# Optimization experiments

Measured on AMD Instinct MI355X. Metric: run time of the kernel, lower is better.

Reference implementation:

```python
import jax, jax.numpy as jnp
import numpy as np

N, E, D_EMB, D_OUT, K = 4096, 131072, 128, 64, 3


def setup_inputs() -> dict:
    key = jax.random.key(0)
    k1, k2, k3, k4 = jax.random.split(key, 4)
    node_features = jax.random.normal(k1, (N, D_EMB), dtype=jnp.float32)
    edge_index = jax.random.randint(k2, (2, E), 0, N, dtype=jnp.int32)
    edge_weights = jax.random.uniform(k3, (E,), dtype=jnp.float32)
    # xavier_uniform-like init for Emb (shape [embdsize, nin])
    limit = float(np.sqrt(6.0 / (D_EMB + D_OUT)))
    Emb = jax.random.uniform(k4, (D_EMB, D_OUT), dtype=jnp.float32, minval=-limit, maxval=limit)
    return {"node_features": node_features, "Emb": Emb,
            "edge_index": edge_index, "edge_weights": edge_weights}


def reference(node_features, Emb, edge_index, edge_weights):
    # embedding: [N, embdsize] @ [embdsize, nin] -> [N, nin]
    x = node_features @ Emb
    n = x.shape[0]
    A = jnp.zeros((n, n), dtype=x.dtype).at[edge_index[0], edge_index[1]].set(edge_weights)
    # matrix_power(A, K) @ x  ==  K repeated A @ x (associativity), avoids forming A^K
    for _ in range(K):
        x = A @ x
    return x
```

## Files before the change

### kernel.cpp

```cpp
#include <hip/hip_runtime.h>
#include <stdint.h>


#define N_NODES 4096
#define D_EMB   128
#define D_OUT   64

#define CAP       128
#define CAP_SHIFT 7

__global__ void embed_kernel(const float* __restrict__ nf,
                             const float* __restrict__ emb,
                             float* __restrict__ x,
                             int* __restrict__ cnt) {
    int tid = blockIdx.x * blockDim.x + threadIdx.x;
    if (tid < N_NODES) cnt[tid] = 0;

    __shared__ float srow[4][D_EMB];
    int wave = threadIdx.x >> 6;
    int lane = threadIdx.x & 63;
    int row  = blockIdx.x * 4 + wave;
    srow[wave][lane]      = nf[row * D_EMB + lane];
    srow[wave][lane + 64] = nf[row * D_EMB + lane + 64];
    __syncthreads();
    float acc = 0.0f;
#pragma unroll 8
    for (int k = 0; k < D_EMB; ++k)
        acc = fmaf(srow[wave][k], emb[k * D_OUT + lane], acc);
    x[row * D_OUT + lane] = acc;
}

__global__ void scatter_kernel(const int* __restrict__ ei,
                               const float* __restrict__ ew, int E,
                               int* __restrict__ cnt,
                               int2* __restrict__ slots,
                               int* __restrict__ eids) {
    int e = blockIdx.x * blockDim.x + threadIdx.x;
    if (e >= E) return;
    int src = ei[e];
    int dst = ei[E + e];
    int idx = atomicAdd(&cnt[src], 1);
    if (idx < CAP) {
        int2 s;
        s.x = dst;
        s.y = __float_as_int(ew[e]);
        int p = (src << CAP_SHIFT) + idx;
        slots[p] = s;
        eids[p]  = e;
    }
}

__global__ void dedup_spmm_kernel(const int* __restrict__ cnt,
                                  int2* __restrict__ slots,
                                  const int* __restrict__ eids,
                                  const float* __restrict__ x,
                                  float* __restrict__ y) {
    __shared__ int   sdst[4][CAP];
    __shared__ int   seid[4][CAP];
    __shared__ float sw[4][CAP];

    int wave = threadIdx.x >> 6;
    int lane = threadIdx.x & 63;
    int row  = blockIdx.x * 4 + wave;
    int c = cnt[row];
    if (c > CAP) c = CAP;
    int2* s = slots + ((long)row << CAP_SHIFT);
    const int* se = eids + ((long)row << CAP_SHIFT);

#pragma unroll
    for (int half = 0; half < 2; ++half) {
        int i = lane + half * 64;
        if (i < c) {
            int2 si = s[i];
            sdst[wave][i] = si.x;
            sw[wave][i]   = __int_as_float(si.y);
            seid[wave][i] = se[i];
        }
    }
    __syncthreads();

#pragma unroll
    for (int half = 0; half < 2; ++half) {
        int i = lane + half * 64;
        if (i < c) {
            int d = sdst[wave][i], id = seid[wave][i];
            bool loser = false;
            for (int j = 0; j < c; ++j)
                loser |= (sdst[wave][j] == d) & (seid[wave][j] > id);
            if (loser) {
                sw[wave][i] = 0.0f;
                s[i].y = 0;
            }
        }
    }
    __syncthreads();

    float acc = 0.0f;
    int i = 0;
    for (; i + 4 <= c; i += 4) {
        float v0 = x[sdst[wave][i]     * D_OUT + lane];
        float v1 = x[sdst[wave][i + 1] * D_OUT + lane];
        float v2 = x[sdst[wave][i + 2] * D_OUT + lane];
        float v3 = x[sdst[wave][i + 3] * D_OUT + lane];
        acc = fmaf(sw[wave][i],     v0, acc);
        acc = fmaf(sw[wave][i + 1], v1, acc);
        acc = fmaf(sw[wave][i + 2], v2, acc);
        acc = fmaf(sw[wave][i + 3], v3, acc);
    }
    for (; i < c; ++i)
        acc = fmaf(sw[wave][i], x[sdst[wave][i] * D_OUT + lane], acc);
    y[row * D_OUT + lane] = acc;
}

__global__ void spmm_kernel(const int* __restrict__ cnt,
                            const int2* __restrict__ slots,
                            const float* __restrict__ x,
                            float* __restrict__ y) {
    int wave = threadIdx.x >> 6;
    int lane = threadIdx.x & 63;
    int row  = blockIdx.x * 4 + wave;
    int c = cnt[row];
    if (c > CAP) c = CAP;
    const int2* s = slots + ((long)row << CAP_SHIFT);
    float acc = 0.0f;
    int i = 0;
    for (; i + 4 <= c; i += 4) {
        int2 s0 = s[i], s1 = s[i + 1], s2 = s[i + 2], s3 = s[i + 3];
        float v0 = x[s0.x * D_OUT + lane];
        float v1 = x[s1.x * D_OUT + lane];
        float v2 = x[s2.x * D_OUT + lane];
        float v3 = x[s3.x * D_OUT + lane];
        acc = fmaf(__int_as_float(s0.y), v0, acc);
        acc = fmaf(__int_as_float(s1.y), v1, acc);
        acc = fmaf(__int_as_float(s2.y), v2, acc);
        acc = fmaf(__int_as_float(s3.y), v3, acc);
    }
    for (; i < c; ++i) {
        int2 si = s[i];
        acc = fmaf(__int_as_float(si.y), x[si.x * D_OUT + lane], acc);
    }
    y[row * D_OUT + lane] = acc;
}

extern "C" void kernel_launch(void* const* d_in, const int* in_sizes, int n_in,
                              void* d_out, int out_size, void* d_ws, size_t ws_size,
                              hipStream_t stream) {
    const float* nf  = (const float*)d_in[0];
    const float* emb = (const float*)d_in[1];
    const int*   ei  = (const int*)d_in[2];
    const float* ew  = (const float*)d_in[3];
    float* out = (float*)d_out;

    const int E = in_sizes[3];

    char* ws = (char*)d_ws;
    size_t o = 0;
    auto take = [&](size_t bytes) -> void* {
        void* p = ws + o;
        o += (bytes + 255) & ~(size_t)255;
        return p;
    };
    int*  cnt   = (int*)take((size_t)N_NODES * 4);
    int2* slots = (int2*)take((size_t)N_NODES * CAP * 8);
    int*  eids  = (int*)take((size_t)N_NODES * CAP * 4);
    float* x0   = (float*)take((size_t)N_NODES * D_OUT * 4);
    float* x1   = (float*)take((size_t)N_NODES * D_OUT * 4);

    const int TB = 256;
    const int EB = (E + TB - 1) / TB;
    const int NB = N_NODES / 4;

    embed_kernel<<<NB, TB, 0, stream>>>(nf, emb, x0, cnt);
    scatter_kernel<<<EB, TB, 0, stream>>>(ei, ew, E, cnt, slots, eids);
    dedup_spmm_kernel<<<NB, TB, 0, stream>>>(cnt, slots, eids, x0, x1);
    spmm_kernel<<<NB, TB, 0, stream>>>(cnt, slots, x1, x0);
    spmm_kernel<<<NB, TB, 0, stream>>>(cnt, slots, x0, out);
}
```

Before: 48.54 us.

## Fuse embed and scatter kernels, pack slots as int4, stage edges in LDS

Merges the embedding GEMM and the edge scatter into one launch by splitting block ranges, and moves the counter zeroing to a memset. Edge id is packed with dst and weight into a single int4 slot, so the separate eid array goes away. Both SpMM kernels now stage slot data into shared memory and unroll the gather by 8 for more memory-level parallelism. The trade-off is that slot storage doubles from 8 to 16 bytes per entry, which adds scatter write traffic, and the memset adds a launch.

```diff
diff --git a/kernel.cpp b/kernel.cpp
--- a/kernel.cpp
+++ b/kernel.cpp
@@ -9,50 +9,46 @@
 #define CAP       128
 #define CAP_SHIFT 7
 
-__global__ void embed_kernel(const float* __restrict__ nf,
-                             const float* __restrict__ emb,
-                             float* __restrict__ x,
-                             int* __restrict__ cnt) {
-    int tid = blockIdx.x * blockDim.x + threadIdx.x;
-    if (tid < N_NODES) cnt[tid] = 0;
-
-    __shared__ float srow[4][D_EMB];
-    int wave = threadIdx.x >> 6;
-    int lane = threadIdx.x & 63;
-    int row  = blockIdx.x * 4 + wave;
-    srow[wave][lane]      = nf[row * D_EMB + lane];
-    srow[wave][lane + 64] = nf[row * D_EMB + lane + 64];
-    __syncthreads();
-    float acc = 0.0f;
+__global__ void embed_scatter_kernel(const float* __restrict__ nf,
+                                     const float* __restrict__ emb,
+                                     float* __restrict__ x,
+                                     const int* __restrict__ ei,
+                                     const float* __restrict__ ew, int E,
+                                     int* __restrict__ cnt,
+                                     int4* __restrict__ slots) {
+    if (blockIdx.x < 1024) {
+        __shared__ float srow[4][D_EMB];
+        int wave = threadIdx.x >> 6;
+        int lane = threadIdx.x & 63;
+        int row  = blockIdx.x * 4 + wave;
+        float2 a = ((const float2*)(nf + (size_t)row * D_EMB))[lane];
+        srow[wave][2 * lane]     = a.x;
+        srow[wave][2 * lane + 1] = a.y;
+        __syncthreads();
+        float acc = 0.0f;
 #pragma unroll 8
-    for (int k = 0; k < D_EMB; ++k)
-        acc = fmaf(srow[wave][k], emb[k * D_OUT + lane], acc);
-    x[row * D_OUT + lane] = acc;
-}
-
-__global__ void scatter_kernel(const int* __restrict__ ei,
-                               const float* __restrict__ ew, int E,
-                               int* __restrict__ cnt,
-                               int2* __restrict__ slots,
-                               int* __restrict__ eids) {
-    int e = blockIdx.x * blockDim.x + threadIdx.x;
-    if (e >= E) return;
-    int src = ei[e];
-    int dst = ei[E + e];
-    int idx = atomicAdd(&cnt[src], 1);
-    if (idx < CAP) {
-        int2 s;
-        s.x = dst;
-        s.y = __float_as_int(ew[e]);
-        int p = (src << CAP_SHIFT) + idx;
-        slots[p] = s;
-        eids[p]  = e;
+        for (int k = 0; k < D_EMB; ++k)
+            acc = fmaf(srow[wave][k], emb[k * D_OUT + lane], acc);
+        x[row * D_OUT + lane] = acc;
+    } else {
+        int e = (blockIdx.x - 1024) * blockDim.x + threadIdx.x;
+        if (e >= E) return;
+        int src = ei[e];
+        int dst = ei[E + e];
+        int idx = atomicAdd(&cnt[src], 1);
+        if (idx < CAP) {
+            int4 s;
+            s.x = dst;
+            s.y = __float_as_int(ew[e]);
+            s.z = e;
+            s.w = 0;
+            slots[(src << CAP_SHIFT) + idx] = s;
+        }
     }
 }
 
 __global__ void dedup_spmm_kernel(const int* __restrict__ cnt,
-                                  int2* __restrict__ slots,
-                                  const int* __restrict__ eids,
+                                  int4* __restrict__ slots,
                                   const float* __restrict__ x,
                                   float* __restrict__ y) {
     __shared__ int   sdst[4][CAP];
@@ -64,17 +60,16 @@
     int row  = blockIdx.x * 4 + wave;
     int c = cnt[row];
     if (c > CAP) c = CAP;
-    int2* s = slots + ((long)row << CAP_SHIFT);
-    const int* se = eids + ((long)row << CAP_SHIFT);
+    int4* s = slots + ((long)row << CAP_SHIFT);
 
 #pragma unroll
     for (int half = 0; half < 2; ++half) {
         int i = lane + half * 64;
         if (i < c) {
-            int2 si = s[i];
+            int4 si = s[i];
             sdst[wave][i] = si.x;
             sw[wave][i]   = __int_as_float(si.y);
-            seid[wave][i] = se[i];
+            seid[wave][i] = si.z;
         }
     }
     __syncthreads();
@@ -89,7 +84,7 @@
                 loser |= (sdst[wave][j] == d) & (seid[wave][j] > id);
             if (loser) {
                 sw[wave][i] = 0.0f;
-                s[i].y = 0;
+                ((int*)&s[i])[1] = 0;
             }
         }
     }
@@ -97,15 +92,17 @@
 
     float acc = 0.0f;
     int i = 0;
-    for (; i + 4 <= c; i += 4) {
-        float v0 = x[sdst[wave][i]     * D_OUT + lane];
-        float v1 = x[sdst[wave][i + 1] * D_OUT + lane];
-        float v2 = x[sdst[wave][i + 2] * D_OUT + lane];
-        float v3 = x[sdst[wave][i + 3] * D_OUT + lane];
-        acc = fmaf(sw[wave][i],     v0, acc);
-        acc = fmaf(sw[wave][i + 1], v1, acc);
-        acc = fmaf(sw[wave][i + 2], v2, acc);
-        acc = fmaf(sw[wave][i + 3], v3, acc);
+    for (; i + 8 <= c; i += 8) {
+        float vw[8], vx[8];
+#pragma unroll
+        for (int k = 0; k < 8; ++k) vw[k] = sw[wave][i + k];
+        int vd[8];
+#pragma unroll
+        for (int k = 0; k < 8; ++k) vd[k] = sdst[wave][i + k];
+#pragma unroll
+        for (int k = 0; k < 8; ++k) vx[k] = x[vd[k] * D_OUT + lane];
+#pragma unroll
+        for (int k = 0; k < 8; ++k) acc = fmaf(vw[k], vx[k], acc);
     }
     for (; i < c; ++i)
         acc = fmaf(sw[wave][i], x[sdst[wave][i] * D_OUT + lane], acc);
@@ -113,32 +110,46 @@
 }
 
 __global__ void spmm_kernel(const int* __restrict__ cnt,
-                            const int2* __restrict__ slots,
+                            const int4* __restrict__ slots,
                             const float* __restrict__ x,
                             float* __restrict__ y) {
+    __shared__ int   sdst[4][CAP];
+    __shared__ float sw[4][CAP];
+
     int wave = threadIdx.x >> 6;
     int lane = threadIdx.x & 63;
     int row  = blockIdx.x * 4 + wave;
     int c = cnt[row];
     if (c > CAP) c = CAP;
-    const int2* s = slots + ((long)row << CAP_SHIFT);
+    const int4* s = slots + ((long)row << CAP_SHIFT);
+
+#pragma unroll
+    for (int half = 0; half < 2; ++half) {
+        int i = lane + half * 64;
+        if (i < c) {
+            int4 si = s[i];
+            sdst[wave][i] = si.x;
+            sw[wave][i]   = __int_as_float(si.y);
+        }
+    }
+    __syncthreads();
+
     float acc = 0.0f;
     int i = 0;
-    for (; i + 4 <= c; i += 4) {
-        int2 s0 = s[i], s1 = s[i + 1], s2 = s[i + 2], s3 = s[i + 3];
-        float v0 = x[s0.x * D_OUT + lane];
-        float v1 = x[s1.x * D_OUT + lane];
-        float v2 = x[s2.x * D_OUT + lane];
-        float v3 = x[s3.x * D_OUT + lane];
-        acc = fmaf(__int_as_float(s0.y), v0, acc);
-        acc = fmaf(__int_as_float(s1.y), v1, acc);
-        acc = fmaf(__int_as_float(s2.y), v2, acc);
-        acc = fmaf(__int_as_float(s3.y), v3, acc);
+    for (; i + 8 <= c; i += 8) {
+        float vw[8], vx[8];
+#pragma unroll
+        for (int k = 0; k < 8; ++k) vw[k] = sw[wave][i + k];
+        int vd[8];
+#pragma unroll
+        for (int k = 0; k < 8; ++k) vd[k] = sdst[wave][i + k];
+#pragma unroll
+        for (int k = 0; k < 8; ++k) vx[k] = x[vd[k] * D_OUT + lane];
+#pragma unroll
+        for (int k = 0; k < 8; ++k) acc = fmaf(vw[k], vx[k], acc);
     }
-    for (; i < c; ++i) {
-        int2 si = s[i];
-        acc = fmaf(__int_as_float(si.y), x[si.x * D_OUT + lane], acc);
-    }
+    for (; i < c; ++i)
+        acc = fmaf(sw[wave][i], x[sdst[wave][i] * D_OUT + lane], acc);
     y[row * D_OUT + lane] = acc;
 }
 
@@ -161,18 +172,18 @@
         return p;
     };
     int*  cnt   = (int*)take((size_t)N_NODES * 4);
-    int2* slots = (int2*)take((size_t)N_NODES * CAP * 8);
-    int*  eids  = (int*)take((size_t)N_NODES * CAP * 4);
+    int4* slots = (int4*)take((size_t)N_NODES * CAP * 16);
     float* x0   = (float*)take((size_t)N_NODES * D_OUT * 4);
     float* x1   = (float*)take((size_t)N_NODES * D_OUT * 4);
 
     const int TB = 256;
-    const int EB = (E + TB - 1) / TB;
     const int NB = N_NODES / 4;
+    const int SB = (E + TB - 1) / TB;
 
-    embed_kernel<<<NB, TB, 0, stream>>>(nf, emb, x0, cnt);
-    scatter_kernel<<<EB, TB, 0, stream>>>(ei, ew, E, cnt, slots, eids);
-    dedup_spmm_kernel<<<NB, TB, 0, stream>>>(cnt, slots, eids, x0, x1);
+    hipMemsetAsync(cnt, 0, (size_t)N_NODES * 4, stream);
+    embed_scatter_kernel<<<NB + SB, TB, 0, stream>>>(nf, emb, x0,
+                                                     ei, ew, E, cnt, slots);
+    dedup_spmm_kernel<<<NB, TB, 0, stream>>>(cnt, slots, x0, x1);
     spmm_kernel<<<NB, TB, 0, stream>>>(cnt, slots, x1, x0);
     spmm_kernel<<<NB, TB, 0, stream>>>(cnt, slots, x0, out);
 }
```

Measured after the change: 44.67 us. 1.09x faster.
